# Kernel optimization log

Measured on AMD Instinct MI355X. Metric: run time of the kernel, lower is better.

The kernel has to match this reference:

```python
import jax, jax.numpy as jnp
import numpy as np

WS, OWS, NH, DIM, MLP_H = 16, 24, 6, 180, 360
PAD = (OWS - WS) // 2
SCALE = (DIM // NH) ** -0.5


def _ln(x, w, b):
    m = jnp.mean(x, -1, keepdims=True)
    v = jnp.var(x, -1, keepdims=True)
    return (x - m) * jax.lax.rsqrt(v + 1e-5) * w + b


def _rpi():
    # relative position index between ordinary (WS) and extended (OWS) windows
    ci = np.stack(np.meshgrid(np.arange(WS), np.arange(WS), indexing='ij')).reshape(2, -1)
    ce = np.stack(np.meshgrid(np.arange(OWS), np.arange(OWS), indexing='ij')).reshape(2, -1)
    rel = (ce[:, None, :] - ci[:, :, None]).transpose(1, 2, 0) + (WS - 1)  # [WS^2, OWS^2, 2]
    rel[:, :, 0] *= WS + OWS - 1
    return jnp.asarray(rel.sum(-1), dtype=jnp.int32)  # values in [0, (WS+OWS-1)^2)


def setup_inputs():
    key = jax.random.key(0)
    ks = jax.random.split(key, 8)
    h = w = 256
    b = 1
    p = lambda k, shape: jax.random.normal(k, shape, jnp.float32) * 0.02
    return {
        'x': jax.random.normal(ks[0], (b, h * w, DIM), jnp.float32),
        'rpi': _rpi(),
        'norm1_w': jnp.ones((DIM,), jnp.float32), 'norm1_b': jnp.zeros((DIM,), jnp.float32),
        'qkv_w': p(ks[1], (DIM, 3 * DIM)), 'qkv_b': jnp.zeros((3 * DIM,), jnp.float32),
        'rpb': p(ks[2], ((WS + OWS - 1) ** 2, NH)),
        'proj_w': p(ks[3], (DIM, DIM)), 'proj_b': jnp.zeros((DIM,), jnp.float32),
        'norm2_w': jnp.ones((DIM,), jnp.float32), 'norm2_b': jnp.zeros((DIM,), jnp.float32),
        'fc1_w': p(ks[4], (DIM, MLP_H)), 'fc1_b': jnp.zeros((MLP_H,), jnp.float32),
        'fc2_w': p(ks[5], (MLP_H, DIM)), 'fc2_b': jnp.zeros((DIM,), jnp.float32),
        'h': h, 'w': w,
    }


def _ocab(x, rpi, norm1_w, norm1_b, qkv_w, qkv_b, rpb, proj_w, proj_b,
          norm2_w, norm2_b, fc1_w, fc1_b, fc2_w, fc2_b, h, w):
    b, L, c = x.shape
    nhw, nww = h // WS, w // WS
    nw = nhw * nww
    shortcut = x
    xn = _ln(x, norm1_w, norm1_b).reshape(b, h, w, c)
    qkv = xn @ qkv_w + qkv_b                      # [b,h,w,3c]
    q = qkv[..., :c]
    kv = jnp.moveaxis(qkv[..., c:], -1, 1)        # [b,2c,h,w]
    # non-overlapping query windows -> [b*nw, WS*WS, c]
    qw = q.reshape(b, nhw, WS, nww, WS, c).transpose(0, 1, 3, 2, 4, 5).reshape(b * nw, WS * WS, c)
    # overlapping KV windows (torch.nn.Unfold(kernel=OWS, stride=WS, pad=PAD) equivalent)
    kv_pad = jnp.pad(kv, ((0, 0), (0, 0), (PAD, PAD), (PAD, PAD)))
    rows = (jnp.arange(nhw) * WS)[:, None] + jnp.arange(OWS)   # [nhw, OWS]
    cols = (jnp.arange(nww) * WS)[:, None] + jnp.arange(OWS)   # [nww, OWS]
    kvw = kv_pad[:, :, rows][:, :, :, :, cols]    # [b,2c,nhw,OWS,nww,OWS]
    kvw = kvw.reshape(b, 2, c, nhw, OWS, nww, OWS)
    kvw = kvw.transpose(1, 0, 3, 5, 4, 6, 2).reshape(2, b * nw, OWS * OWS, c)
    k_w, v_w = kvw[0], kvw[1]
    B_, nq, n, d = b * nw, WS * WS, OWS * OWS, c // NH
    q_ = qw.reshape(B_, nq, NH, d).transpose(0, 2, 1, 3) * SCALE
    k_ = k_w.reshape(B_, n, NH, d).transpose(0, 2, 1, 3)
    v_ = v_w.reshape(B_, n, NH, d).transpose(0, 2, 1, 3)
    attn = jnp.einsum('bhqd,bhnd->bhqn', q_, k_)
    bias = rpb[rpi.reshape(-1)].reshape(nq, n, NH).transpose(2, 0, 1)  # [NH, nq, n]
    attn = jax.nn.softmax(attn + bias[None], axis=-1)
    out = jnp.einsum('bhqn,bhnd->bhqd', attn, v_).transpose(0, 2, 1, 3).reshape(B_, nq, c)
    # window reverse
    out = out.reshape(b, nhw, nww, WS, WS, c).transpose(0, 1, 3, 2, 4, 5).reshape(b, h * w, c)
    x = out @ proj_w + proj_b + shortcut
    xn2 = _ln(x, norm2_w, norm2_b)
    mlp = jax.nn.gelu(xn2 @ fc1_w + fc1_b, approximate=False) @ fc2_w + fc2_b
    return x + mlp


def reference(x, rpi, norm1_w, norm1_b, qkv_w, qkv_b, rpb, proj_w, proj_b,
              norm2_w, norm2_b, fc1_w, fc1_b, fc2_w, fc2_b, h, w):
    return _ocab(x, rpi, norm1_w, norm1_b, qkv_w, qkv_b, rpb, proj_w, proj_b,
                 norm2_w, norm2_b, fc1_w, fc1_b, fc2_w, fc2_b, h, w)
```

## Files before the change

kernel.cpp:

```cpp
#include <hip/hip_runtime.h>

typedef float f32x4 __attribute__((ext_vector_type(4)));
typedef float fvec4 __attribute__((ext_vector_type(4)));
typedef __bf16 bf16x8 __attribute__((ext_vector_type(8)));
typedef unsigned short u16;
typedef u16 u16x8 __attribute__((ext_vector_type(8)));
typedef u16 u16x4 __attribute__((ext_vector_type(4)));
typedef int i32x2 __attribute__((ext_vector_type(2)));

#define SCALE_Q 0.18257418583505536f
#define LOG2E   1.4426950408889634f
#define SCALE_Q2 (SCALE_Q * LOG2E)

__device__ __forceinline__ u16 f2bf(float f) {
    union { __bf16 h; u16 u; } cv; cv.h = (__bf16)f; return cv.u;
}
__device__ __forceinline__ float bf2f(u16 u) {
    union { __bf16 h; u16 u; } cv; cv.u = u; return (float)cv.h;
}
__device__ __forceinline__ float exp2_raw(float x) {
    float r;
    asm("v_exp_f32 %0, %1" : "=v"(r) : "v"(x));
    return r;
}
__device__ __forceinline__ unsigned pk_bf16(float a, float b) {
    unsigned r;
    asm("v_cvt_pk_bf16_f32 %0, %1, %2" : "=v"(r) : "v"(a), "v"(b));
    return r;
}

#define GLD16(gsrc, ldst) __builtin_amdgcn_global_load_lds( \
    (const __attribute__((address_space(1))) unsigned*)(gsrc), \
    (__attribute__((address_space(3))) unsigned*)(ldst), 16, 0, 0)

__device__ __forceinline__ void xswap16(int a, int b, int& u, int& v) {
#if __has_builtin(__builtin_amdgcn_permlane16_swap)
    i32x2 r = __builtin_amdgcn_permlane16_swap(a, b, false, false);
    u = r[0]; v = r[1];
#else
    int sa = __builtin_amdgcn_ds_swizzle(a, 0x401F);
    int sb = __builtin_amdgcn_ds_swizzle(b, 0x401F);
    bool hi = (threadIdx.x & 16) != 0;
    u = hi ? sb : a;
    v = hi ? b : sa;
#endif
}

__device__ __forceinline__ void border_yx(int i, int& y, int& x) {
    if (i < 1056)      { y = i / 264; x = i % 264; }
    else if (i < 2112) { int j = i - 1056; y = 260 + j / 264; x = j % 264; }
    else               { int j = i - 2112; y = 4 + (j >> 3); int xx = j & 7;
                         x = (xx < 4) ? xx : 256 + xx; }
}

__global__ __launch_bounds__(256)
void prepln_k(const float* __restrict__ x, const float* __restrict__ n1w,
              const float* __restrict__ n1b, u16* __restrict__ xn,
              const float* __restrict__ qkv_w, const float* __restrict__ proj_w,
              const float* __restrict__ fc1_w, const float* __restrict__ fc2_w,
              const int* __restrict__ rpi, const float* __restrict__ rpb,
              u16* __restrict__ qkvT, u16* __restrict__ projT,
              u16* __restrict__ fc1T, u16* __restrict__ fc2T,
              u16* __restrict__ bias5, unsigned* __restrict__ kp_u32,
              unsigned* __restrict__ vp_u32)
{
    if (blockIdx.x < 16384) {
        int row = blockIdx.x * 4 + (threadIdx.x >> 6);
        int lane = threadIdx.x & 63;
        fvec4 v = {0.f, 0.f, 0.f, 0.f};
        if (lane < 45) v = *(const fvec4*)(x + (long)row * 180 + lane * 4);
        float s  = v.x + v.y + v.z + v.w;
        float sq = v.x * v.x + v.y * v.y + v.z * v.z + v.w * v.w;
        for (int m = 1; m < 64; m <<= 1) { s += __shfl_xor(s, m); sq += __shfl_xor(sq, m); }
        float mean = s * (1.f / 180.f);
        float var  = sq * (1.f / 180.f) - mean * mean;
        float rstd = rsqrtf(var + 1e-5f);
        if (lane < 45) {
            u16x4 o;
            #pragma unroll
            for (int j = 0; j < 4; j++) {
                int c = lane * 4 + j;
                o[j] = f2bf((v[j] - mean) * rstd * n1w[c] + n1b[c]);
            }
            *(u16x4*)(xn + (long)row * 192 + lane * 4) = o;
        } else if (lane < 48) {
            u16x4 z = {0, 0, 0, 0};
            *(u16x4*)(xn + (long)row * 192 + 180 + (lane - 45) * 4) = z;
        }
        return;
    }
    int idx = (blockIdx.x - 16384) * 256 + threadIdx.x;
    if (idx < 122880) {
        int e = idx & 7, l15b = (idx >> 3) & 15, lgb = (idx >> 7) & 3;
        int kstep = (idx >> 9) % 6, ng = idx / 3072;
        int col = ng * 16 + l15b, kd = kstep * 32 + lgb * 8 + e;
        qkvT[idx] = (col < 540 && kd < 180) ? f2bf(qkv_w[kd * 540 + col]) : (u16)0;
    } else if (idx < 172032) {
        int i = idx - 122880;
        int e = i & 7, l15b = (i >> 3) & 15, lgb = (i >> 7) & 3;
        int kstep = (i >> 9) % 6, ng = i / 3072;
        int col = ng * 16 + l15b, kd = kstep * 32 + lgb * 8 + e;
        projT[i] = (col < 180 && kd < 180) ? f2bf(proj_w[kd * 180 + col]) : (u16)0;
    } else if (idx < 245760) {
        int i = idx - 172032;
        int e = i & 7, l15b = (i >> 3) & 15, lgb = (i >> 7) & 3;
        int kstep = (i >> 9) % 6, ng = i / 3072;
        int col = ng * 16 + l15b, kd = kstep * 32 + lgb * 8 + e;
        fc1T[i] = (col < 360 && kd < 180) ? f2bf(fc1_w[kd * 360 + col]) : (u16)0;
    } else if (idx < 344064) {
        int i = idx - 245760;
        int e = i & 7, l15b = (i >> 3) & 15, lgb = (i >> 7) & 3;
        int kstep = (i >> 9) % 12, ng = i / 6144;
        int col = ng * 16 + l15b, kd = kstep * 32 + lgb * 8 + e;
        fc2T[i] = (col < 180 && kd < 360) ? f2bf(fc2_w[kd * 180 + col]) : (u16)0;
    } else if (idx < 1228800) {
        int i = idx - 344064;
        int e = i & 15, l15 = (i >> 4) & 15, wv2 = (i >> 8) & 3, lg2 = (i >> 10) & 3;
        int cm36 = i >> 12;
        int hh = cm36 / 36, cm = cm36 % 36;
        int ch = cm >> 2, mi = cm & 3;
        int ni = e >> 2, rr = e & 3;
        int q = wv2 * 64 + ni * 16 + l15;
        int key = ch * 64 + mi * 16 + lg2 * 4 + rr;
        bias5[i] = f2bf(rpb[rpi[q * 576 + key] * 6 + hh] * LOG2E);
    } else if (idx < 1628160) {
        int i = idx - 1228800;
        int tok = i >> 4, wj = i & 15;
        int h = tok / 4160, b = tok % 4160, y, xx;
        border_yx(b, y, xx);
        kp_u32[((h * 264 + y) * 264 + xx) * 16 + wj] = 0u;
    } else if (idx < 2021376) {
        int i = idx - 1628160;
        int h = i / 65536, t = i % 65536;
        int y = t >> 8, xx = t & 255;
        kp_u32[((h * 264 + y + 4) * 264 + xx + 4) * 16 + 15] = 0u;
    } else if (idx < 2236800) {
        int i = idx - 2021376;
        int h = i / 35904, r = i % 35904;
        vp_u32[(h * 32 + 30) * 35904 + r] = 0x3F803F80u;
    } else if (idx < 2452224) {
        int i = idx - 2236800;
        int h = i / 35904, r = i % 35904;
        vp_u32[(h * 32 + 31) * 35904 + r] = 0u;
    } else if (idx < 3016704) {
        int i = idx - 2452224;
        int hd = i / 3136, j = i % 3136;
        int h = hd / 30, d = hd % 30;
        int y, xu;
        if (j < 1088) { int r = j / 136; y = r + (r >= 4 ? 256 : 0); xu = j % 136; }
        else { int j2 = j - 1088; y = 4 + (j2 >> 3); int q = j2 & 7;
               xu = (q < 2) ? q : 128 + q; }
        vp_u32[((h * 32 + d) * 264 + y) * 136 + xu] = 0u;
    }
}

__global__ __launch_bounds__(256)
void lnb_k(const u16* __restrict__ in, const float* __restrict__ w,
           const float* __restrict__ b, u16* __restrict__ out)
{
    int row = blockIdx.x * 4 + (threadIdx.x >> 6);
    int lane = threadIdx.x & 63;
    fvec4 v = {0.f, 0.f, 0.f, 0.f};
    if (lane < 45) {
        u16x4 raw = *(const u16x4*)(in + (long)row * 192 + lane * 4);
        #pragma unroll
        for (int j = 0; j < 4; j++) v[j] = bf2f(raw[j]);
    }
    float s  = v.x + v.y + v.z + v.w;
    float sq = v.x * v.x + v.y * v.y + v.z * v.z + v.w * v.w;
    for (int m = 1; m < 64; m <<= 1) { s += __shfl_xor(s, m); sq += __shfl_xor(sq, m); }
    float mean = s * (1.f / 180.f);
    float var  = sq * (1.f / 180.f) - mean * mean;
    float rstd = rsqrtf(var + 1e-5f);
    if (lane < 45) {
        u16x4 o;
        #pragma unroll
        for (int j = 0; j < 4; j++) {
            int c = lane * 4 + j;
            o[j] = f2bf((v[j] - mean) * rstd * w[c] + b[c]);
        }
        *(u16x4*)(out + (long)row * 192 + lane * 4) = o;
    } else if (lane < 48) {
        u16x4 z = {0, 0, 0, 0};
        *(u16x4*)(out + (long)row * 192 + 180 + (lane - 45) * 4) = z;
    }
}

template<int KTOT, int NCB, int EPI>
__global__ __launch_bounds__(256)
void gemm_k(const u16* __restrict__ A, const u16* __restrict__ BtF,
            const float* __restrict__ bias, const float* __restrict__ resid,
            void* __restrict__ o0, void* __restrict__ o1, void* __restrict__ o2)
{
    constexpr int NKT = KTOT / 32;
    __shared__ u16 lds_a[128 * 192];
    const int tid = threadIdx.x;
    const int l = tid & 63, wv = tid >> 6;
    const int wm = wv >> 1, wn = wv & 1;
    const int l15 = l & 15, lg = l >> 4;
    const int rx7 = l15 & 7;
    const long rowb = (long)blockIdx.x * 128;
    const int cb0 = blockIdx.y * NCB;
    const f32x4 fz = {0.f, 0.f, 0.f, 0.f};

    f32x4 acc[4][2];
    #pragma unroll
    for (int i = 0; i < 4; i++) { acc[i][0] = fz; acc[i][1] = fz; }

    const u16* aptr[4];
    #pragma unroll
    for (int mi = 0; mi < 4; mi++)
        aptr[mi] = lds_a + (wm * 64 + mi * 16 + l15) * 192;

    auto epilogue = [&](int cb, f32x4 (&ac)[4][2]) {
        #pragma unroll
        for (int nd = 0; nd < 2; nd++) {
            const int c = cb * 64 + wn * 32 + nd * 16 + l15;
            if (EPI == 0) {
                if (c < 540) {
                    const float bb = bias[c];
                    const int sec = (c >= 360) ? 2 : ((c >= 180) ? 1 : 0);
                    const int cc = c - sec * 180;
                    const int hh = cc / 30, d = cc - hh * 30;
                    #pragma unroll
                    for (int mi = 0; mi < 4; mi++) {
                        const long t0 = rowb + wm * 64 + mi * 16 + lg * 4;
                        const int y = (int)(t0 >> 8), x0 = (int)(t0 & 255);
                        if (sec == 0) {
                            int win = ((y >> 4) << 4) | (x0 >> 4);
                            int qrow0 = ((y & 15) << 4) | (x0 & 15);
                            u16* dst = (u16*)o0 + (((long)(win * 6 + hh)) * 256 + qrow0) * 32 + d;
                            #pragma unroll
                            for (int rr = 0; rr < 4; rr++)
                                dst[rr * 32] = f2bf((ac[mi][nd][rr] + bb) * SCALE_Q2);
                        } else if (sec == 1) {
                            u16* dst = (u16*)o1 + (((long)hh * 264 + y + 4) * 264 + x0 + 4) * 32 + d;
                            #pragma unroll
                            for (int rr = 0; rr < 4; rr++)
                                dst[rr * 32] = f2bf(ac[mi][nd][rr] + bb);
                        } else {
                            long dstoff = (((long)hh * 32 + d) * 264 + y + 4) * 272 + x0 + 4;
                            union { u16x4 v4; unsigned u2[2]; } pv;
                            pv.u2[0] = pk_bf16(ac[mi][nd][0] + bb, ac[mi][nd][1] + bb);
                            pv.u2[1] = pk_bf16(ac[mi][nd][2] + bb, ac[mi][nd][3] + bb);
                            *(u16x4*)((u16*)o2 + dstoff) = pv.v4;
                        }
                    }
                }
            } else {
                if (c < 180) {
                    const float bb = bias[c];
                    #pragma unroll
                    for (int mi = 0; mi < 4; mi++) {
                        const long t0 = rowb + wm * 64 + mi * 16 + lg * 4;
                        const float* rs = resid + t0 * 180 + c;
                        u16* dst = (u16*)o0 + t0 * 192 + c;
                        #pragma unroll
                        for (int rr = 0; rr < 4; rr++)
                            dst[rr * 192] = f2bf(ac[mi][nd][rr] + bb + rs[rr * 180]);
                    }
                }
            }
        }
    };

    #pragma unroll
    for (int R = 0; R < 12; ++R) {
        int idx = R * 256 + tid;
        int row = idx / 24, gp = idx - row * 24;
        int g = (gp & 24) | ((gp & 7) ^ (row & 7));
        GLD16(A + (rowb + row) * KTOT + g * 8,
              (char*)lds_a + R * 4096 + wv * 1024);
    }
    __syncthreads();

    #pragma unroll
    for (int icb = 0; icb < NCB; ++icb) {
        const u16* Bf = BtF + ((long)((cb0 + icb) * 4 + wn * 2) * NKT) * 512 + l * 8;
        #pragma unroll
        for (int kg = 0; kg < 6; kg += 3) {
            bf16x8 bfr[2][3];
            #pragma unroll
            for (int g2 = 0; g2 < 3; ++g2) {
                bfr[0][g2] = *(const bf16x8*)(Bf + (kg + g2) * 512);
                bfr[1][g2] = *(const bf16x8*)(Bf + (NKT + kg + g2) * 512);
            }
            #pragma unroll
            for (int g2 = 0; g2 < 3; ++g2) {
                const int k = kg + g2;
                const int gk = k * 4 + lg;
                const int gpk = (gk & 24) | ((gk & 7) ^ rx7);
                bf16x8 af[4];
                #pragma unroll
                for (int mi = 0; mi < 4; mi++)
                    af[mi] = *(const bf16x8*)(aptr[mi] + gpk * 8);
                #pragma unroll
                for (int mi = 0; mi < 4; mi++)
                    #pragma unroll
                    for (int nd = 0; nd < 2; nd++)
                        acc[mi][nd] = __builtin_amdgcn_mfma_f32_16x16x32_bf16(af[mi], bfr[nd][g2], acc[mi][nd], 0, 0, 0);
            }
        }
        epilogue(cb0 + icb, acc);
        #pragma unroll
        for (int i = 0; i < 4; i++) { acc[i][0] = fz; acc[i][1] = fz; }
    }
}

__global__ __launch_bounds__(256)
void mlp_k(const u16* __restrict__ A, const u16* __restrict__ fc1T,
           const u16* __restrict__ fc2T, const float* __restrict__ b1,
           const float* __restrict__ b2, const u16* __restrict__ resid,
           float* __restrict__ out)
{
    __shared__ u16 lds_a[64 * 192];
    __shared__ u16 H[64 * 384];
    const int tid = threadIdx.x;
    const int l = tid & 63, wv = tid >> 6;
    const int l15 = l & 15, lg = l >> 4;
    const int rx7 = l15 & 7;
    const long rowb = (long)blockIdx.x * 64;
    const f32x4 fz = {0.f, 0.f, 0.f, 0.f};

    #pragma unroll
    for (int R = 0; R < 6; ++R) {
        int idx = R * 256 + tid;
        int row = idx / 24, gp = idx - row * 24;
        int g = (gp & 24) | ((gp & 7) ^ (row & 7));
        GLD16(A + (rowb + row) * 192 + g * 8, (char*)lds_a + R * 4096 + wv * 1024);
    }
    __syncthreads();

    const u16* aptr[4];
    #pragma unroll
    for (int mi = 0; mi < 4; mi++)
        aptr[mi] = lds_a + (mi * 16 + l15) * 192;

    #pragma unroll
    for (int cb = 0; cb < 6; ++cb) {
        f32x4 ac[4] = {fz, fz, fz, fz};
        const u16* Bf = fc1T + ((long)(cb * 4 + wv) * 6) * 512 + l * 8;
        #pragma unroll
        for (int k = 0; k < 6; ++k) {
            bf16x8 bfr = *(const bf16x8*)(Bf + k * 512);
            const int gk = k * 4 + lg;
            const int gpk = (gk & 24) | ((gk & 7) ^ rx7);
            bf16x8 af[4];
            #pragma unroll
            for (int mi = 0; mi < 4; mi++)
                af[mi] = *(const bf16x8*)(aptr[mi] + gpk * 8);
            #pragma unroll
            for (int mi = 0; mi < 4; mi++)
                ac[mi] = __builtin_amdgcn_mfma_f32_16x16x32_bf16(af[mi], bfr, ac[mi], 0, 0, 0);
        }
        const int c = cb * 64 + wv * 16 + l15;
        const float bb = (c < 360) ? b1[c] : 0.f;
        const int gC = c >> 3, cL = c & 7;
        #pragma unroll
        for (int mi = 0; mi < 4; mi++) {
            #pragma unroll
            for (int rr = 0; rr < 4; rr++) {
                int row = mi * 16 + lg * 4 + rr;
                float xx = ac[mi][rr] + bb;
                float u2n = -2.f * xx * (0.7978845608f + 0.0356774081f * xx * xx);
                float ge = xx / (1.f + __expf(u2n));
                int gS = (gC & ~7) | ((gC & 7) ^ (row & 7));
                H[row * 384 + gS * 8 + cL] = f2bf(ge);
            }
        }
    }
    __syncthreads();

    #pragma unroll
    for (int cb = 0; cb < 3; ++cb) {
        f32x4 ac[4] = {fz, fz, fz, fz};
        const u16* Bf = fc2T + ((long)(cb * 4 + wv) * 12) * 512 + l * 8;
        #pragma unroll
        for (int k = 0; k < 12; ++k) {
            bf16x8 bfr = *(const bf16x8*)(Bf + k * 512);
            const int gk = k * 4 + lg;
            const int gS = (gk & ~7) | ((gk & 7) ^ rx7);
            bf16x8 af[4];
            #pragma unroll
            for (int mi = 0; mi < 4; mi++)
                af[mi] = *(const bf16x8*)(H + (mi * 16 + l15) * 384 + gS * 8);
            #pragma unroll
            for (int mi = 0; mi < 4; mi++)
                ac[mi] = __builtin_amdgcn_mfma_f32_16x16x32_bf16(af[mi], bfr, ac[mi], 0, 0, 0);
        }
        const int c = cb * 64 + wv * 16 + l15;
        if (c < 180) {
            const float bb = b2[c];
            #pragma unroll
            for (int mi = 0; mi < 4; mi++) {
                const long t0 = rowb + mi * 16 + lg * 4;
                const u16* rs = resid + t0 * 192 + c;
                float* dst = out + t0 * 180 + c;
                #pragma unroll
                for (int rr = 0; rr < 4; rr++)
                    dst[rr * 180] = ac[mi][rr] + bb + bf2f(rs[rr * 192]);
            }
        }
    }
}

__global__ __launch_bounds__(256)
void attn_k(const u16* __restrict__ q_g, const u16* __restrict__ K_pad,
            const u16* __restrict__ vP, const u16* __restrict__ bias5,
            u16* __restrict__ attn_out)
{
    __shared__ u16 kc[2][64 * 32];
    __shared__ u16 vt[2][32 * 64];

    const int w = ((blockIdx.x & 7) << 5) | (blockIdx.x >> 3);
    const int h = blockIdx.y;
    const int wy = w >> 4, wx = w & 15;
    const int tid = threadIdx.x;
    const int wv = tid >> 6, l = tid & 63;
    const int l15 = l & 15, lg = l >> 4;
    const int swzk = (l15 >> 1) & 3;
    const int swzv = l15 & 7;

    bf16x8 qb[4];
    #pragma unroll
    for (int ni = 0; ni < 4; ni++) {
        int qrow = wv * 64 + ni * 16 + l15;
        qb[ni] = *(const bf16x8*)(q_g + (((long)(w * 6 + h)) * 256 + qrow) * 32 + lg * 8);
    }

    f32x4 acc[2][4];
    #pragma unroll
    for (int i = 0; i < 2; i++)
        #pragma unroll
        for (int j = 0; j < 4; j++) acc[i][j] = (f32x4){0.f, 0.f, 0.f, 0.f};

    const int tK = tid >> 2;
    const int gtk = (l & 3) ^ ((l >> 3) & 3);
    const int aK = (tK >= 48) ? 2 : (tK >= 24 ? 1 : 0);
    const int bK = tK - aK * 24;
    const u16* KbaseRow = K_pad + (((long)(h * 264 + wy * 16)) * 264 + wx * 16) * 32 + gtk * 8;
    const int dV = tid >> 3;
    const int gtv = (l & 7) ^ (l >> 3);
    const int aV = gtv / 3, bV = (gtv % 3) * 8;
    const u16* Vrow0 = vP + ((((long)h * 32 + dV) * 264) + wy * 16) * 272 + wx * 16;
    const u16* Bp = bias5 + (long)h * 147456 + ((lg * 4 + wv) * 16 + l15) * 16;

    GLD16(KbaseRow + ((long)aK * 264 + bK) * 32, (char*)kc[0] + wv * 1024);
    GLD16(Vrow0 + aV * 272 + bV, (char*)vt[0] + wv * 1024);

    u16x8 bl[4], bh[4];
    #pragma unroll
    for (int mi = 0; mi < 4; mi++) {
        bl[mi] = *(const u16x8*)(Bp + mi * 4096);
        bh[mi] = *(const u16x8*)(Bp + mi * 4096 + 8);
    }

    #pragma unroll
    for (int ch = 0; ch < 9; ++ch) {
        __syncthreads();
        u16x8 bln[4], bhn[4];
        if (ch < 8) {
            int n = (ch + 1) * 64;
            int c1 = n / 24, c2 = n - c1 * 24;
            int bb2 = bK + c2;
            int t2 = bb2 >= 24;
            int oy = c1 + aK + t2, ox = bb2 - (t2 ? 24 : 0);
            GLD16(KbaseRow + ((long)oy * 264 + ox) * 32, (char*)kc[(ch + 1) & 1] + wv * 1024);
            int bbv = bV + c2;
            int t2v = bbv >= 24;
            int oyv = c1 + aV + t2v, oxv = bbv - (t2v ? 24 : 0);
            GLD16(Vrow0 + oyv * 272 + oxv, (char*)vt[(ch + 1) & 1] + wv * 1024);
            #pragma unroll
            for (int mi = 0; mi < 4; mi++) {
                bln[mi] = *(const u16x8*)(Bp + ((ch + 1) * 4 + mi) * 4096);
                bhn[mi] = *(const u16x8*)(Bp + ((ch + 1) * 4 + mi) * 4096 + 8);
            }
        }
        const u16* kcur = kc[ch & 1];
        const u16* vcur = vt[ch & 1];

        #pragma unroll
        for (int ks = 0; ks < 2; ++ks) {
            int Wp[2][4][2];
            #pragma unroll
            for (int mih = 0; mih < 2; ++mih) {
                int mi = ks * 2 + mih;
                int key = ks * 32 + mih * 16 + l15;
                bf16x8 ka = *(const bf16x8*)(kcur + key * 32 + (lg ^ swzk) * 8);
                union { u16x8 v; unsigned d[4]; } ulo, uhi;
                ulo.v = bl[mi]; uhi.v = bh[mi];
                f32x4 s[4];
                #pragma unroll
                for (int ni = 0; ni < 4; ni++) {
                    unsigned dA = (ni < 2) ? ulo.d[(ni & 1) * 2]     : uhi.d[(ni & 1) * 2];
                    unsigned dB = (ni < 2) ? ulo.d[(ni & 1) * 2 + 1] : uhi.d[(ni & 1) * 2 + 1];
                    f32x4 ci;
                    ci[0] = __uint_as_float(dA << 16);
                    ci[1] = __uint_as_float(dA & 0xFFFF0000u);
                    ci[2] = __uint_as_float(dB << 16);
                    ci[3] = __uint_as_float(dB & 0xFFFF0000u);
                    s[ni] = ci;
                }
                #pragma unroll
                for (int ni = 0; ni < 4; ni++)
                    s[ni] = __builtin_amdgcn_mfma_f32_16x16x32_bf16(ka, qb[ni], s[ni], 0, 0, 0);
                #pragma unroll
                for (int ni = 0; ni < 4; ni++) {
                    float p0 = exp2_raw(s[ni][0]);
                    float p1 = exp2_raw(s[ni][1]);
                    float p2 = exp2_raw(s[ni][2]);
                    float p3 = exp2_raw(s[ni][3]);
                    Wp[mih][ni][0] = (int)pk_bf16(p0, p1);
                    Wp[mih][ni][1] = (int)pk_bf16(p2, p3);
                }
            }
            bf16x8 va0 = *(const bf16x8*)(vcur + l15 * 64 + ((ks * 4 + lg) ^ swzv) * 8);
            bf16x8 va1 = *(const bf16x8*)(vcur + (16 + l15) * 64 + ((ks * 4 + lg) ^ swzv) * 8);
            #pragma unroll
            for (int ni = 0; ni < 4; ni++) {
                i32x2 r0 = __builtin_amdgcn_permlane32_swap(Wp[0][ni][0], Wp[1][ni][0], false, false);
                i32x2 r1 = __builtin_amdgcn_permlane32_swap(Wp[0][ni][1], Wp[1][ni][1], false, false);
                int wd0, wd1, wd2, wd3;
                xswap16(r0[0], r0[1], wd0, wd2);
                xswap16(r1[0], r1[1], wd1, wd3);
                union { int wd[4]; bf16x8 v; } pu;
                pu.wd[0] = wd0; pu.wd[1] = wd1; pu.wd[2] = wd2; pu.wd[3] = wd3;
                acc[0][ni] = __builtin_amdgcn_mfma_f32_16x16x32_bf16(va0, pu.v, acc[0][ni], 0, 0, 0);
                acc[1][ni] = __builtin_amdgcn_mfma_f32_16x16x32_bf16(va1, pu.v, acc[1][ni], 0, 0, 0);
            }
        }
        if (ch < 8) {
            #pragma unroll
            for (int mi = 0; mi < 4; mi++) { bl[mi] = bln[mi]; bh[mi] = bhn[mi]; }
        }
    }

    #pragma unroll
    for (int ni = 0; ni < 4; ni++) {
        float sum = __shfl(acc[1][ni][2], 48 + l15);
        float inv = 1.f / sum;
        int q = wv * 64 + ni * 16 + l15;
        int y = wy * 16 + (q >> 4), x = wx * 16 + (q & 15);
        u16* bp = attn_out + ((long)(y * 256 + x)) * 192 + h * 30;
        unsigned w0 = pk_bf16(acc[0][ni][0] * inv, acc[0][ni][1] * inv);
        unsigned w1 = pk_bf16(acc[0][ni][2] * inv, acc[0][ni][3] * inv);
        *(unsigned*)(bp + lg * 4)     = w0;
        *(unsigned*)(bp + lg * 4 + 2) = w1;
        unsigned w2 = pk_bf16(acc[1][ni][0] * inv, acc[1][ni][1] * inv);
        if (lg < 3) {
            unsigned w3 = pk_bf16(acc[1][ni][2] * inv, acc[1][ni][3] * inv);
            *(unsigned*)(bp + 16 + lg * 4)     = w2;
            *(unsigned*)(bp + 16 + lg * 4 + 2) = w3;
        } else {
            *(unsigned*)(bp + 28) = w2;
        }
    }
}

extern "C" void kernel_launch(void* const* d_in, const int* in_sizes, int n_in,
                              void* d_out, int out_size, void* d_ws, size_t ws_size,
                              hipStream_t stream)
{
    (void)in_sizes; (void)n_in; (void)out_size; (void)ws_size;
    const float* x      = (const float*)d_in[0];
    const int*   rpi    = (const int*)d_in[1];
    const float* n1w    = (const float*)d_in[2];
    const float* n1b    = (const float*)d_in[3];
    const float* qkv_w  = (const float*)d_in[4];
    const float* qkv_b  = (const float*)d_in[5];
    const float* rpb    = (const float*)d_in[6];
    const float* proj_w = (const float*)d_in[7];
    const float* proj_b = (const float*)d_in[8];
    const float* n2w    = (const float*)d_in[9];
    const float* n2b    = (const float*)d_in[10];
    const float* fc1_w  = (const float*)d_in[11];
    const float* fc1_b  = (const float*)d_in[12];
    const float* fc2_w  = (const float*)d_in[13];
    const float* fc2_b  = (const float*)d_in[14];
    float* out = (float*)d_out;

    char* ws = (char*)d_ws;
    size_t off = 0;
    auto alloc = [&](size_t bytes) -> void* {
        void* p = ws + off; off += (bytes + 511) & ~(size_t)511; return p;
    };
    u16*   xn     = (u16*)alloc(65536ull * 192 * 2);
    u16*   q_g    = (u16*)alloc(65536ull * 192 * 2);
    u16*   K_pad  = (u16*)alloc(6ull * 264 * 264 * 32 * 2);
    u16*   x2b    = (u16*)alloc(65536ull * 192 * 2);
    u16*   vP     = (u16*)alloc(6ull * 32 * 264 * 272 * 2);
    u16*   bias5  = (u16*)alloc(6ull * 36 * 4 * 4 * 16 * 16 * 2);
    u16*   qkvT   = (u16*)alloc(640ull * 192 * 2);
    u16*   projT  = (u16*)alloc(256ull * 192 * 2);
    u16*   fc1T   = (u16*)alloc(384ull * 192 * 2);
    u16*   fc2T   = (u16*)alloc(256ull * 384 * 2);
    u16*   ao     = xn;
    u16*   xn2    = q_g;

    prepln_k<<<dim3(28168), dim3(256), 0, stream>>>(x, n1w, n1b, xn,
        qkv_w, proj_w, fc1_w, fc2_w, rpi, rpb,
        qkvT, projT, fc1T, fc2T, bias5, (unsigned*)K_pad, (unsigned*)vP);
    gemm_k<192, 3, 0><<<dim3(512, 3), dim3(256), 0, stream>>>(
        xn, qkvT, qkv_b, (const float*)nullptr, q_g, K_pad, vP);
    attn_k<<<dim3(256, 6), dim3(256), 0, stream>>>(q_g, K_pad, vP, bias5, ao);
    gemm_k<192, 3, 1><<<dim3(512, 1), dim3(256), 0, stream>>>(
        ao, projT, proj_b, x, x2b, nullptr, nullptr);
    lnb_k<<<dim3(16384), dim3(256), 0, stream>>>(x2b, n2w, n2b, xn2);
    mlp_k<<<dim3(1024), dim3(256), 0, stream>>>(
        xn2, fc1T, fc2T, fc1_b, fc2_b, x2b, out);
}
```

Before: 218.7 us.

## Fuse LayerNorm2 into MLP kernel and pad attention output heads to 32

```diff
diff --git a/kernel.cpp b/kernel.cpp
--- a/kernel.cpp
+++ b/kernel.cpp
@@ -99,8 +99,10 @@
         int i = idx - 122880;
         int e = i & 7, l15b = (i >> 3) & 15, lgb = (i >> 7) & 3;
         int kstep = (i >> 9) % 6, ng = i / 3072;
-        int col = ng * 16 + l15b, kd = kstep * 32 + lgb * 8 + e;
-        projT[i] = (col < 180 && kd < 180) ? f2bf(proj_w[kd * 180 + col]) : (u16)0;
+        int col = ng * 16 + l15b, kdp = kstep * 32 + lgb * 8 + e;
+        int sub = kdp & 31;
+        int k = (kdp >> 5) * 30 + sub;
+        projT[i] = (col < 180 && sub < 30) ? f2bf(proj_w[k * 180 + col]) : (u16)0;
     } else if (idx < 245760) {
         int i = idx - 172032;
         int e = i & 7, l15b = (i >> 3) & 15, lgb = (i >> 7) & 3;
@@ -154,38 +156,6 @@
     }
 }
 
-__global__ __launch_bounds__(256)
-void lnb_k(const u16* __restrict__ in, const float* __restrict__ w,
-           const float* __restrict__ b, u16* __restrict__ out)
-{
-    int row = blockIdx.x * 4 + (threadIdx.x >> 6);
-    int lane = threadIdx.x & 63;
-    fvec4 v = {0.f, 0.f, 0.f, 0.f};
-    if (lane < 45) {
-        u16x4 raw = *(const u16x4*)(in + (long)row * 192 + lane * 4);
-        #pragma unroll
-        for (int j = 0; j < 4; j++) v[j] = bf2f(raw[j]);
-    }
-    float s  = v.x + v.y + v.z + v.w;
-    float sq = v.x * v.x + v.y * v.y + v.z * v.z + v.w * v.w;
-    for (int m = 1; m < 64; m <<= 1) { s += __shfl_xor(s, m); sq += __shfl_xor(sq, m); }
-    float mean = s * (1.f / 180.f);
-    float var  = sq * (1.f / 180.f) - mean * mean;
-    float rstd = rsqrtf(var + 1e-5f);
-    if (lane < 45) {
-        u16x4 o;
-        #pragma unroll
-        for (int j = 0; j < 4; j++) {
-            int c = lane * 4 + j;
-            o[j] = f2bf((v[j] - mean) * rstd * w[c] + b[c]);
-        }
-        *(u16x4*)(out + (long)row * 192 + lane * 4) = o;
-    } else if (lane < 48) {
-        u16x4 z = {0, 0, 0, 0};
-        *(u16x4*)(out + (long)row * 192 + 180 + (lane - 45) * 4) = z;
-    }
-}
-
 template<int KTOT, int NCB, int EPI>
 __global__ __launch_bounds__(256)
 void gemm_k(const u16* __restrict__ A, const u16* __restrict__ BtF,
@@ -259,6 +229,15 @@
                         for (int rr = 0; rr < 4; rr++)
                             dst[rr * 192] = f2bf(ac[mi][nd][rr] + bb + rs[rr * 180]);
                     }
+                } else {
+                    #pragma unroll
+                    for (int mi = 0; mi < 4; mi++) {
+                        const long t0 = rowb + wm * 64 + mi * 16 + lg * 4;
+                        u16* dst = (u16*)o0 + t0 * 192 + c;
+                        #pragma unroll
+                        for (int rr = 0; rr < 4; rr++)
+                            dst[rr * 192] = 0;
+                    }
                 }
             }
         }
@@ -308,10 +287,10 @@
 }
 
 __global__ __launch_bounds__(256)
-void mlp_k(const u16* __restrict__ A, const u16* __restrict__ fc1T,
+void mlp_k(const u16* __restrict__ x2b, const u16* __restrict__ fc1T,
            const u16* __restrict__ fc2T, const float* __restrict__ b1,
-           const float* __restrict__ b2, const u16* __restrict__ resid,
-           float* __restrict__ out)
+           const float* __restrict__ b2, const float* __restrict__ n2w,
+           const float* __restrict__ n2b, float* __restrict__ out)
 {
     __shared__ u16 lds_a[64 * 192];
     __shared__ u16 H[64 * 384];
@@ -327,7 +306,47 @@
         int idx = R * 256 + tid;
         int row = idx / 24, gp = idx - row * 24;
         int g = (gp & 24) | ((gp & 7) ^ (row & 7));
-        GLD16(A + (rowb + row) * 192 + g * 8, (char*)lds_a + R * 4096 + wv * 1024);
+        GLD16(x2b + (rowb + row) * 192 + g * 8, (char*)lds_a + R * 4096 + wv * 1024);
+    }
+    __syncthreads();
+
+    {
+        const int row = tid >> 2, q = tid & 3;
+        const int rw7 = row & 7;
+        u16* rbase = lds_a + row * 192;
+        u16x8 vals[6];
+        float s = 0.f, sq = 0.f;
+        #pragma unroll
+        for (int j = 0; j < 6; ++j) {
+            int g = q * 6 + j;
+            int pg = (g & 24) | ((g & 7) ^ rw7);
+            vals[j] = *(const u16x8*)(rbase + pg * 8);
+            #pragma unroll
+            for (int e = 0; e < 8; ++e) {
+                float v = bf2f(vals[j][e]);
+                s += v; sq += v * v;
+            }
+        }
+        s  += __shfl_xor(s, 1);  sq += __shfl_xor(sq, 1);
+        s  += __shfl_xor(s, 2);  sq += __shfl_xor(sq, 2);
+        float mean = s * (1.f / 180.f);
+        float var  = sq * (1.f / 180.f) - mean * mean;
+        float rstd = rsqrtf(var + 1e-5f);
+        #pragma unroll
+        for (int j = 0; j < 6; ++j) {
+            int g = q * 6 + j;
+            int pg = (g & 24) | ((g & 7) ^ rw7);
+            u16x8 o;
+            #pragma unroll
+            for (int e = 0; e < 8; ++e) {
+                int c = g * 8 + e;
+                int cc = (c < 180) ? c : 0;
+                float v = bf2f(vals[j][e]);
+                float nv = (v - mean) * rstd * n2w[cc] + n2b[cc];
+                o[e] = (c < 180) ? f2bf(nv) : (u16)0;
+            }
+            *(u16x8*)(rbase + pg * 8) = o;
+        }
     }
     __syncthreads();
 
@@ -394,7 +413,7 @@
             #pragma unroll
             for (int mi = 0; mi < 4; mi++) {
                 const long t0 = rowb + mi * 16 + lg * 4;
-                const u16* rs = resid + t0 * 192 + c;
+                const u16* rs = x2b + t0 * 192 + c;
                 float* dst = out + t0 * 180 + c;
                 #pragma unroll
                 for (int rr = 0; rr < 4; rr++)
@@ -541,18 +560,15 @@
         float inv = 1.f / sum;
         int q = wv * 64 + ni * 16 + l15;
         int y = wy * 16 + (q >> 4), x = wx * 16 + (q & 15);
-        u16* bp = attn_out + ((long)(y * 256 + x)) * 192 + h * 30;
-        unsigned w0 = pk_bf16(acc[0][ni][0] * inv, acc[0][ni][1] * inv);
-        unsigned w1 = pk_bf16(acc[0][ni][2] * inv, acc[0][ni][3] * inv);
-        *(unsigned*)(bp + lg * 4)     = w0;
-        *(unsigned*)(bp + lg * 4 + 2) = w1;
-        unsigned w2 = pk_bf16(acc[1][ni][0] * inv, acc[1][ni][1] * inv);
+        u16* bp = attn_out + ((long)(y * 256 + x)) * 192 + h * 32;
+        *(unsigned*)(bp + lg * 4)     = pk_bf16(acc[0][ni][0] * inv, acc[0][ni][1] * inv);
+        *(unsigned*)(bp + lg * 4 + 2) = pk_bf16(acc[0][ni][2] * inv, acc[0][ni][3] * inv);
         if (lg < 3) {
-            unsigned w3 = pk_bf16(acc[1][ni][2] * inv, acc[1][ni][3] * inv);
-            *(unsigned*)(bp + 16 + lg * 4)     = w2;
-            *(unsigned*)(bp + 16 + lg * 4 + 2) = w3;
+            *(unsigned*)(bp + 16 + lg * 4)     = pk_bf16(acc[1][ni][0] * inv, acc[1][ni][1] * inv);
+            *(unsigned*)(bp + 16 + lg * 4 + 2) = pk_bf16(acc[1][ni][2] * inv, acc[1][ni][3] * inv);
         } else {
-            *(unsigned*)(bp + 28) = w2;
+            *(unsigned*)(bp + 28) = pk_bf16(acc[1][ni][0] * inv, acc[1][ni][1] * inv);
+            *(unsigned*)(bp + 30) = 0u;
         }
     }
 }
@@ -595,7 +611,6 @@
     u16*   fc1T   = (u16*)alloc(384ull * 192 * 2);
     u16*   fc2T   = (u16*)alloc(256ull * 384 * 2);
     u16*   ao     = xn;
-    u16*   xn2    = q_g;
 
     prepln_k<<<dim3(28168), dim3(256), 0, stream>>>(x, n1w, n1b, xn,
         qkv_w, proj_w, fc1_w, fc2_w, rpi, rpb,
@@ -605,7 +620,6 @@
     attn_k<<<dim3(256, 6), dim3(256), 0, stream>>>(q_g, K_pad, vP, bias5, ao);
     gemm_k<192, 3, 1><<<dim3(512, 1), dim3(256), 0, stream>>>(
         ao, projT, proj_b, x, x2b, nullptr, nullptr);
-    lnb_k<<<dim3(16384), dim3(256), 0, stream>>>(x2b, n2w, n2b, xn2);
     mlp_k<<<dim3(1024), dim3(256), 0, stream>>>(
-        xn2, fc1T, fc2T, fc1_b, fc2_b, x2b, out);
-}
+        x2b, fc1T, fc2T, fc1_b, fc2_b, n2w, n2b, out);
+}
```

Result: faster. 209.9 us (median of 3 runs) (-4.0%).
